# Performance work log

Measured on AMD Instinct MI355X. Metric: run time of the kernel, lower is better.

The kernel has to match this reference:

```python
import jax, jax.numpy as jnp
import numpy as np

CH = 512          # channels
HEADS = 8
HEAD_CH = 64
HIDDEN = HEADS * HEAD_CH  # 512
GROUPS = 32
EPS = 1e-5


def setup_inputs() -> dict:
    key = jax.random.key(0)
    ks = jax.random.split(key, 6)
    x = jax.random.normal(ks[0], (16, 32, 32, CH), dtype=jnp.float32)
    gn_scale = jnp.ones((CH,), dtype=jnp.float32)
    gn_offset = jnp.zeros((CH,), dtype=jnp.float32)
    w_qkv = jax.random.normal(ks[1], (CH, 3 * HIDDEN), dtype=jnp.float32) * 0.02
    # out_proj is zero-init in the original; use small random weights so the
    # residual branch is non-trivial for kernel correctness testing.
    w_out = jax.random.normal(ks[2], (HIDDEN, CH), dtype=jnp.float32) * 0.02
    b_out = jax.random.normal(ks[3], (CH,), dtype=jnp.float32) * 0.02
    return {"x": x, "gn_scale": gn_scale, "gn_offset": gn_offset,
            "w_qkv": w_qkv, "w_out": w_out, "b_out": b_out}


def group_norm(x, scale, offset):
    b, h, w, c = x.shape
    xg = x.reshape(b, h, w, GROUPS, c // GROUPS)
    mean = jnp.mean(xg, axis=(1, 2, 4), keepdims=True)
    var = jnp.var(xg, axis=(1, 2, 4), keepdims=True)
    xg = (xg - mean) * jax.lax.rsqrt(var + EPS)
    return xg.reshape(b, h, w, c) * scale + offset


def reference(x, gn_scale, gn_offset, w_qkv, w_out, b_out):
    b, h, w, c = x.shape
    n = h * w
    xn = jax.nn.silu(group_norm(x, gn_scale, gn_offset))
    qkv = jnp.einsum('bxyc,cd->bxyd', xn, w_qkv)  # [b,h,w,3*hidden]
    q, k, v = jnp.split(qkv, 3, axis=-1)
    # 'b x y (h c) -> b h c (x y)'
    def to_heads(a):
        a = a.reshape(b, n, HEADS, HEAD_CH)
        return jnp.transpose(a, (0, 2, 3, 1))  # b h d n
    q, k, v = to_heads(q), to_heads(k), to_heads(v)
    q = q * (HEAD_CH ** -0.5)
    sim = jnp.einsum('bhdi,bhdj->bhij', q, k)
    attn = jax.nn.softmax(sim, axis=-1)  # stable softmax (matches max-subtract)
    out = jnp.einsum('bhij,bhdj->bhid', attn, v)  # b h n d
    # 'b h (x y) d -> b x y (h d)'
    out = jnp.transpose(out, (0, 2, 1, 3)).reshape(b, h_ := h, w, HIDDEN) if False else \
          jnp.transpose(out, (0, 2, 1, 3)).reshape(b, h, w, HIDDEN)
    out = jnp.einsum('bxyd,dc->bxyc', out, w_out) + b_out
    return out + x
```

## Files before the change

### kernel.cpp

```cpp
#include <hip/hip_runtime.h>

#define BATCH 16
#define NPIX 1024
#define CH 512
#define HEADS 8
#define HD 64
#define GROUPS 32
#define CG 16
#define QKVW 1536

using bf16x8 = __attribute__((ext_vector_type(8))) short;
using f32x4  = __attribute__((ext_vector_type(4))) float;

__device__ inline unsigned short f2bf(float f) {
  unsigned int u = __builtin_bit_cast(unsigned int, f);
  u += 0x7fffu + ((u >> 16) & 1u);
  return (unsigned short)(u >> 16);
}

__device__ inline unsigned cvtpk(float lo, float hi) {
  unsigned r;
  asm("v_cvt_pk_bf16_f32 %0, %1, %2" : "=v"(r) : "v"(lo), "v"(hi));
  return r;
}

__device__ inline bf16x8 lds_frag(const unsigned short* S, int row, int slot) {
  return *(const bf16x8*)(S + row * 64 + (((slot ^ (row & 7)) << 3)));
}

__device__ inline void gload16(const unsigned short* g, unsigned short* l) {
  __builtin_amdgcn_global_load_lds(
      (const __attribute__((address_space(1))) unsigned int*)g,
      (__attribute__((address_space(3))) unsigned int*)l, 16, 0, 0);
}

__global__ __launch_bounds__(256) void wconv_kernel(
    const float* __restrict__ src, unsigned short* __restrict__ dst,
    const int K, const int N, const int q_cols) {
  __shared__ float tile[64][65];
  const int nb = N >> 6;
  const int k0 = (blockIdx.x / nb) << 6, n0 = (blockIdx.x % nb) << 6;
  const int t = threadIdx.x;
  const int row = t >> 2, c0 = (t & 3) << 4;
#pragma unroll
  for (int j = 0; j < 4; ++j) {
    const float4 v = *reinterpret_cast<const float4*>(
        src + (size_t)(k0 + row) * N + n0 + c0 + j * 4);
    tile[row][c0 + j * 4 + 0] = v.x;
    tile[row][c0 + j * 4 + 1] = v.y;
    tile[row][c0 + j * 4 + 2] = v.z;
    tile[row][c0 + j * 4 + 3] = v.w;
  }
  __syncthreads();
  const int n = t >> 2, kc = (t & 3) << 4;
  const float s = ((n0 + n) < q_cols) ? (0.125f * 1.44269504f) : 1.f;
#pragma unroll
  for (int j = 0; j < 4; ++j) {
    ushort4 o;
    o.x = f2bf(tile[kc + j * 4 + 0][n] * s);
    o.y = f2bf(tile[kc + j * 4 + 1][n] * s);
    o.z = f2bf(tile[kc + j * 4 + 2][n] * s);
    o.w = f2bf(tile[kc + j * 4 + 3][n] * s);
    *reinterpret_cast<ushort4*>(dst + (size_t)(n0 + n) * K + k0 + kc + j * 4) = o;
  }
}

__global__ __launch_bounds__(256) void gn_silu_kernel(
    const float* __restrict__ x, const float* __restrict__ sc,
    const float* __restrict__ of, unsigned short* __restrict__ y) {
  const int b = blockIdx.x >> 5, g = blockIdx.x & 31;
  const size_t base = (size_t)b * NPIX * CH + (size_t)g * CG;
  const int t = threadIdx.x;

  float4 vv[16];
  float sum = 0.f, ssq = 0.f;
#pragma unroll
  for (int it = 0; it < 16; ++it) {
    const int e4 = t + 256 * it;
    const int p = e4 >> 2, c = (e4 & 3) * 4;
    vv[it] = *reinterpret_cast<const float4*>(x + base + (size_t)p * CH + c);
    sum += vv[it].x + vv[it].y + vv[it].z + vv[it].w;
    ssq += vv[it].x * vv[it].x + vv[it].y * vv[it].y +
           vv[it].z * vv[it].z + vv[it].w * vv[it].w;
  }
#pragma unroll
  for (int m = 32; m > 0; m >>= 1) {
    sum += __shfl_down(sum, m);
    ssq += __shfl_down(ssq, m);
  }
  __shared__ float rs[4], rq[4], mv[2];
  const int lane = t & 63, wid = t >> 6;
  if (lane == 0) { rs[wid] = sum; rq[wid] = ssq; }
  __syncthreads();
  if (t == 0) {
    const float s = rs[0] + rs[1] + rs[2] + rs[3];
    const float q = rq[0] + rq[1] + rq[2] + rq[3];
    const float mean = s * (1.f / 16384.f);
    const float var = q * (1.f / 16384.f) - mean * mean;
    mv[0] = mean;
    mv[1] = rsqrtf(var + 1e-5f);
  }
  __syncthreads();
  const float mean = mv[0], rstd = mv[1];

#pragma unroll
  for (int it = 0; it < 16; ++it) {
    const int e4 = t + 256 * it;
    const int p = e4 >> 2, c = (e4 & 3) * 4;
    const float4 s4 = *reinterpret_cast<const float4*>(sc + g * CG + c);
    const float4 o4 = *reinterpret_cast<const float4*>(of + g * CG + c);
    float r[4];
    r[0] = (vv[it].x - mean) * rstd * s4.x + o4.x;
    r[1] = (vv[it].y - mean) * rstd * s4.y + o4.y;
    r[2] = (vv[it].z - mean) * rstd * s4.z + o4.z;
    r[3] = (vv[it].w - mean) * rstd * s4.w + o4.w;
    ushort4 o;
    o.x = f2bf(r[0] / (1.f + __expf(-r[0])));
    o.y = f2bf(r[1] / (1.f + __expf(-r[1])));
    o.z = f2bf(r[2] / (1.f + __expf(-r[2])));
    o.w = f2bf(r[3] / (1.f + __expf(-r[3])));
    *reinterpret_cast<ushort4*>(y + base + (size_t)p * CH + c) = o;
  }
}

template <bool EPI>
__global__ __launch_bounds__(256) void gemm_bf16_kernel(
    const unsigned short* __restrict__ A, const unsigned short* __restrict__ BT,
    void* __restrict__ Cv, const int M, const int N,
    const float* __restrict__ bias, const float* __restrict__ resid,
    unsigned short* __restrict__ vT) {
  __shared__ unsigned short lds[16384];
  unsigned short* As = lds;
  unsigned short* Bs = lds + 8192;
  const int Kd = 512;
  const int t = threadIdx.x;
  int bid = blockIdx.x;
  { const int q = gridDim.x >> 3; bid = (bid & 7) * q + (bid >> 3); }
  const int nb = N >> 7;
  const int m0 = (bid / nb) << 7, n0 = (bid % nb) << 7;
  const int wv = t >> 6, lane = t & 63;
  const int wr = (wv >> 1) << 6, wc = (wv & 1) << 6;
  const int l15 = lane & 15, l4 = lane >> 4;
  const bool vmode = !EPI && (n0 >= 1024);

  const int srow = t >> 3, sslot = t & 7;
  const int gslot = sslot ^ (srow & 7);
  const unsigned short* ag = A + (size_t)(m0 + srow) * Kd + gslot * 8;
  const unsigned short* bg = BT + (size_t)(n0 + srow) * Kd + gslot * 8;
  unsigned short* aw = As + wv * 512;
  unsigned short* bw = Bs + wv * 512;

  f32x4 acc[4][4];
#pragma unroll
  for (int i = 0; i < 4; ++i)
#pragma unroll
    for (int j = 0; j < 4; ++j) acc[i][j] = {0.f, 0.f, 0.f, 0.f};

#pragma unroll
  for (int s = 0; s < 8; ++s) {
    const int k0 = s * 64;
#pragma unroll
    for (int i = 0; i < 4; ++i) {
      gload16(ag + (size_t)(32 * i) * Kd + k0, aw + i * 2048);
      gload16(bg + (size_t)(32 * i) * Kd + k0, bw + i * 2048);
    }
    __syncthreads();
#pragma unroll
    for (int kk = 0; kk < 2; ++kk) {
      bf16x8 af[4], bfr[4];
#pragma unroll
      for (int i = 0; i < 4; ++i) {
        af[i] = lds_frag(As, wr + i * 16 + l15, kk * 4 + l4);
        bfr[i] = lds_frag(Bs, wc + i * 16 + l15, kk * 4 + l4);
      }
      if (vmode) {
#pragma unroll
        for (int ni = 0; ni < 4; ++ni)
#pragma unroll
          for (int mi = 0; mi < 4; ++mi)
            acc[ni][mi] = __builtin_amdgcn_mfma_f32_16x16x32_bf16(
                bfr[ni], af[mi], acc[ni][mi], 0, 0, 0);
      } else {
#pragma unroll
        for (int mi = 0; mi < 4; ++mi)
#pragma unroll
          for (int ni = 0; ni < 4; ++ni)
            acc[mi][ni] = __builtin_amdgcn_mfma_f32_16x16x32_bf16(
                af[mi], bfr[ni], acc[mi][ni], 0, 0, 0);
      }
    }
    __syncthreads();
  }

  if (EPI) {
#pragma unroll
    for (int mi = 0; mi < 4; ++mi)
#pragma unroll
      for (int ni = 0; ni < 4; ++ni) {
        const int col = n0 + wc + ni * 16 + l15;
#pragma unroll
        for (int r = 0; r < 4; ++r) {
          const int row = m0 + wr + mi * 16 + l4 * 4 + r;
          const size_t idx = (size_t)row * N + col;
          ((float*)Cv)[idx] = acc[mi][ni][r] + bias[col] + resid[idx];
        }
      }
  } else {
    unsigned short* Ct = lds;
#pragma unroll
    for (int ii = 0; ii < 4; ++ii)
#pragma unroll
      for (int jj = 0; jj < 4; ++jj) {
        const int rb = vmode ? (wc + ii * 16 + l4 * 4) : (wr + ii * 16 + l4 * 4);
        const int col = vmode ? (wr + jj * 16 + l15) : (wc + jj * 16 + l15);
#pragma unroll
        for (int r = 0; r < 4; ++r) {
          const int row = rb + r;
          Ct[row * 128 + ((((col >> 3) ^ (row & 15))) << 3) + (col & 7)] =
              f2bf(acc[ii][jj][r]);
        }
      }
    __syncthreads();
    const int erow = t >> 4;
    const int eslot = t & 15;
    if (!vmode) {
#pragma unroll
      for (int j = 0; j < 8; ++j) {
        const int row = erow + 16 * j;
        const uint4 v = *reinterpret_cast<const uint4*>(
            Ct + row * 128 + ((eslot ^ (row & 15)) << 3));
        *reinterpret_cast<uint4*>(
            (unsigned short*)Cv + (size_t)(m0 + row) * N + n0 + eslot * 8) = v;
      }
    } else {
      const int bb = m0 >> 10;
#pragma unroll
      for (int j = 0; j < 8; ++j) {
        const int row = erow + 16 * j;
        const uint4 v = *reinterpret_cast<const uint4*>(
            Ct + row * 128 + ((eslot ^ (row & 15)) << 3));
        *reinterpret_cast<uint4*>(
            vT + (((size_t)(bb * 512 + (n0 - 1024) + row)) << 10) +
            (m0 & 1023) + eslot * 8) = v;
      }
    }
  }
}

__global__ __launch_bounds__(256) void attn_mfma_kernel(
    const unsigned short* __restrict__ qkv, const unsigned short* __restrict__ vT,
    unsigned short* __restrict__ outb) {
  __shared__ unsigned short Ks[2][64 * 64];
  __shared__ unsigned short Vt[64 * 64];
  __shared__ unsigned short Ps[128 * 64];

  int bid = blockIdx.x;
  { const int q = gridDim.x >> 3; bid = (bid & 7) * q + (bid >> 3); }
  const int qt = bid & 7, h = (bid >> 3) & 7, b = bid >> 6;
  const int t = threadIdx.x, wv = t >> 6, lane = t & 63;
  const int l15 = lane & 15, l4 = lane >> 4;
  const int q0 = qt * 128;
  const size_t base = (size_t)b * NPIX * QKVW + h * HD;

  bf16x8 qf[2][2];
#pragma unroll
  for (int mi = 0; mi < 2; ++mi)
#pragma unroll
    for (int kk = 0; kk < 2; ++kk) {
      const int row = q0 + wv * 32 + mi * 16 + l15;
      qf[mi][kk] = *reinterpret_cast<const bf16x8*>(
          qkv + base + (size_t)row * QKVW + kk * 32 + l4 * 8);
    }

  f32x4 oaccT[4][2];
#pragma unroll
  for (int i = 0; i < 4; ++i)
#pragma unroll
    for (int j = 0; j < 2; ++j) oaccT[i][j] = {0.f, 0.f, 0.f, 0.f};
  float lrun[2] = {0.f, 0.f};

  const int srow = t >> 3, sslot = t & 7;
  const int gslot = sslot ^ (srow & 7);
  const unsigned short* kgp = qkv + base + 512 + (size_t)srow * QKVW + gslot * 8;
  const unsigned short* vgp =
      vT + (((size_t)(b * 512 + h * HD + srow)) << 10) + gslot * 8;
  unsigned short* kw[2] = {&Ks[0][0] + wv * 512, &Ks[1][0] + wv * 512};
  unsigned short* vw = &Vt[0] + wv * 512;

#pragma unroll
  for (int i = 0; i < 2; ++i) {
    gload16(kgp + (size_t)(32 * i) * QKVW, kw[0] + i * 2048);
    gload16(vgp + ((size_t)(32 * i) << 10), vw + i * 2048);
    gload16(kgp + (size_t)(64 + 32 * i) * QKVW, kw[1] + i * 2048);
  }
  __syncthreads();

  for (int kt = 0; kt < 16; ++kt) {
    const int cur = kt & 1;

    f32x4 sacc[4][2];
#pragma unroll
    for (int i = 0; i < 4; ++i)
#pragma unroll
      for (int j = 0; j < 2; ++j) sacc[i][j] = {0.f, 0.f, 0.f, 0.f};
    __builtin_amdgcn_s_setprio(1);
#pragma unroll
    for (int kk = 0; kk < 2; ++kk) {
      bf16x8 kf[4];
#pragma unroll
      for (int ni = 0; ni < 4; ++ni)
        kf[ni] = lds_frag(&Ks[cur][0], ni * 16 + l15, kk * 4 + l4);
#pragma unroll
      for (int ni = 0; ni < 4; ++ni)
#pragma unroll
        for (int mi = 0; mi < 2; ++mi)
          sacc[ni][mi] = __builtin_amdgcn_mfma_f32_16x16x32_bf16(
              kf[ni], qf[mi][kk], sacc[ni][mi], 0, 0, 0);
    }
    __builtin_amdgcn_s_setprio(0);

#pragma unroll
    for (int mi = 0; mi < 2; ++mi) {
      const int prow = wv * 32 + mi * 16 + l15;
      float rsum = 0.f;
#pragma unroll
      for (int ni = 0; ni < 4; ++ni) {
        float p[4];
#pragma unroll
        for (int r = 0; r < 4; ++r) {
          p[r] = exp2f(sacc[ni][mi][r]);
          rsum += p[r];
        }
        uint2 pw;
        pw.x = cvtpk(p[0], p[1]);
        pw.y = cvtpk(p[2], p[3]);
        const int slot = ni * 2 + (l4 >> 1);
        *reinterpret_cast<uint2*>(
            Ps + prow * 64 + ((slot ^ (prow & 7)) << 3) + ((l4 & 1) << 2)) = pw;
      }
      rsum += __shfl_xor(rsum, 16);
      rsum += __shfl_xor(rsum, 32);
      lrun[mi] += rsum;
    }

    __syncthreads();

    __builtin_amdgcn_s_setprio(1);
#pragma unroll
    for (int kk = 0; kk < 2; ++kk) {
      bf16x8 vf[4], pf[2];
#pragma unroll
      for (int dn = 0; dn < 4; ++dn)
        vf[dn] = lds_frag(&Vt[0], dn * 16 + l15, kk * 4 + l4);
#pragma unroll
      for (int mi = 0; mi < 2; ++mi)
        pf[mi] = lds_frag(Ps, wv * 32 + mi * 16 + l15, kk * 4 + l4);
#pragma unroll
      for (int dn = 0; dn < 4; ++dn)
#pragma unroll
        for (int mi = 0; mi < 2; ++mi)
          oaccT[dn][mi] = __builtin_amdgcn_mfma_f32_16x16x32_bf16(
              vf[dn], pf[mi], oaccT[dn][mi], 0, 0, 0);
    }
    __builtin_amdgcn_s_setprio(0);

    __syncthreads();

    if (kt < 15) {
      const int n0v = (kt + 1) * 64;
#pragma unroll
      for (int i = 0; i < 2; ++i)
        gload16(vgp + ((size_t)(32 * i) << 10) + n0v, vw + i * 2048);
      if (kt < 14) {
        const int n0k = (kt + 2) * 64;
#pragma unroll
        for (int i = 0; i < 2; ++i)
          gload16(kgp + (size_t)(n0k + 32 * i) * QKVW, kw[cur] + i * 2048);
      }
    }
  }

#pragma unroll
  for (int mi = 0; mi < 2; ++mi) {
    const float inv = 1.f / lrun[mi];
    const size_t n = (size_t)b * NPIX + q0 + wv * 32 + mi * 16 + l15;
#pragma unroll
    for (int dn = 0; dn < 4; ++dn) {
      uint2 o;
      o.x = cvtpk(oaccT[dn][mi][0] * inv, oaccT[dn][mi][1] * inv);
      o.y = cvtpk(oaccT[dn][mi][2] * inv, oaccT[dn][mi][3] * inv);
      *reinterpret_cast<uint2*>(outb + n * CH + h * HD + dn * 16 + l4 * 4) = o;
    }
  }
}

extern "C" void kernel_launch(void* const* d_in, const int* in_sizes, int n_in,
                              void* d_out, int out_size, void* d_ws, size_t ws_size,
                              hipStream_t stream) {
  const float* x = (const float*)d_in[0];
  const float* gsc = (const float*)d_in[1];
  const float* gof = (const float*)d_in[2];
  const float* wqkv = (const float*)d_in[3];
  const float* wout = (const float*)d_in[4];
  const float* bout = (const float*)d_in[5];
  float* out = (float*)d_out;

  unsigned short* qkvb = (unsigned short*)d_ws;
  unsigned short* xnb = qkvb + (size_t)16384 * 1536;
  unsigned short* wqT = xnb + (size_t)16384 * 512;
  unsigned short* woT = wqT + (size_t)1536 * 512;
  unsigned short* vTb = woT + (size_t)512 * 512;
  const size_t need = ((size_t)16384 * 1536 + (size_t)16384 * 512 +
                       (size_t)1536 * 512 + (size_t)512 * 512 +
                       (size_t)16 * 512 * 1024) * 2;
  if (ws_size < need) return;

  wconv_kernel<<<(512 / 64) * (1536 / 64), 256, 0, stream>>>(
      wqkv, wqT, 512, 1536, 512);
  wconv_kernel<<<(512 / 64) * (512 / 64), 256, 0, stream>>>(
      wout, woT, 512, 512, 0);
  gn_silu_kernel<<<BATCH * GROUPS, 256, 0, stream>>>(x, gsc, gof, xnb);
  gemm_bf16_kernel<false><<<(16384 / 128) * (1536 / 128), 256, 0, stream>>>(
      xnb, wqT, qkvb, 16384, 1536, nullptr, nullptr, vTb);
  attn_mfma_kernel<<<BATCH * HEADS * 8, 256, 0, stream>>>(qkvb, vTb, xnb);
  gemm_bf16_kernel<true><<<(16384 / 128) * (512 / 128), 256, 0, stream>>>(
      xnb, woT, out, 16384, 512, bout, x, nullptr);
}
```

Baseline: 154.8 us.

## Load K/V fragments directly from global memory, dropping LDS staging and block barriers

After: 207.2 us. 33.9% more time.

```diff
diff --git a/kernel.cpp b/kernel.cpp
--- a/kernel.cpp
+++ b/kernel.cpp
@@ -250,8 +250,6 @@
 __global__ __launch_bounds__(256) void attn_mfma_kernel(
     const unsigned short* __restrict__ qkv, const unsigned short* __restrict__ vT,
     unsigned short* __restrict__ outb) {
-  __shared__ unsigned short Ks[2][64 * 64];
-  __shared__ unsigned short Vt[64 * 64];
   __shared__ unsigned short Ps[128 * 64];
 
   int bid = blockIdx.x;
@@ -272,6 +270,10 @@
           qkv + base + (size_t)row * QKVW + kk * 32 + l4 * 8);
     }
 
+  const unsigned short* kfb = qkv + base + 512 + (size_t)l15 * QKVW + l4 * 8;
+  const unsigned short* vfb =
+      vT + (((size_t)(b * 512 + h * HD + l15)) << 10) + l4 * 8;
+
   f32x4 oaccT[4][2];
 #pragma unroll
   for (int i = 0; i < 4; ++i)
@@ -279,24 +281,16 @@
     for (int j = 0; j < 2; ++j) oaccT[i][j] = {0.f, 0.f, 0.f, 0.f};
   float lrun[2] = {0.f, 0.f};
 
-  const int srow = t >> 3, sslot = t & 7;
-  const int gslot = sslot ^ (srow & 7);
-  const unsigned short* kgp = qkv + base + 512 + (size_t)srow * QKVW + gslot * 8;
-  const unsigned short* vgp =
-      vT + (((size_t)(b * 512 + h * HD + srow)) << 10) + gslot * 8;
-  unsigned short* kw[2] = {&Ks[0][0] + wv * 512, &Ks[1][0] + wv * 512};
-  unsigned short* vw = &Vt[0] + wv * 512;
-
-#pragma unroll
-  for (int i = 0; i < 2; ++i) {
-    gload16(kgp + (size_t)(32 * i) * QKVW, kw[0] + i * 2048);
-    gload16(vgp + ((size_t)(32 * i) << 10), vw + i * 2048);
-    gload16(kgp + (size_t)(64 + 32 * i) * QKVW, kw[1] + i * 2048);
-  }
-  __syncthreads();
-
   for (int kt = 0; kt < 16; ++kt) {
-    const int cur = kt & 1;
+    const int n0k = kt * 64;
+
+    bf16x8 kf[2][4];
+#pragma unroll
+    for (int kk = 0; kk < 2; ++kk)
+#pragma unroll
+      for (int ni = 0; ni < 4; ++ni)
+        kf[kk][ni] = *reinterpret_cast<const bf16x8*>(
+            kfb + (size_t)(n0k + ni * 16) * QKVW + kk * 32);
 
     f32x4 sacc[4][2];
 #pragma unroll
@@ -305,19 +299,22 @@
       for (int j = 0; j < 2; ++j) sacc[i][j] = {0.f, 0.f, 0.f, 0.f};
     __builtin_amdgcn_s_setprio(1);
 #pragma unroll
-    for (int kk = 0; kk < 2; ++kk) {
-      bf16x8 kf[4];
-#pragma unroll
-      for (int ni = 0; ni < 4; ++ni)
-        kf[ni] = lds_frag(&Ks[cur][0], ni * 16 + l15, kk * 4 + l4);
+    for (int kk = 0; kk < 2; ++kk)
 #pragma unroll
       for (int ni = 0; ni < 4; ++ni)
 #pragma unroll
         for (int mi = 0; mi < 2; ++mi)
           sacc[ni][mi] = __builtin_amdgcn_mfma_f32_16x16x32_bf16(
-              kf[ni], qf[mi][kk], sacc[ni][mi], 0, 0, 0);
-    }
+              kf[kk][ni], qf[mi][kk], sacc[ni][mi], 0, 0, 0);
     __builtin_amdgcn_s_setprio(0);
+
+    bf16x8 vf[2][4];
+#pragma unroll
+    for (int kk = 0; kk < 2; ++kk)
+#pragma unroll
+      for (int dn = 0; dn < 4; ++dn)
+        vf[kk][dn] = *reinterpret_cast<const bf16x8*>(
+            vfb + (((size_t)(dn * 16)) << 10) + n0k + kk * 32);
 
 #pragma unroll
     for (int mi = 0; mi < 2; ++mi) {
@@ -343,15 +340,13 @@
       lrun[mi] += rsum;
     }
 
-    __syncthreads();
+    asm volatile("s_waitcnt lgkmcnt(0)" ::: "memory");
+    __builtin_amdgcn_sched_barrier(0);
 
     __builtin_amdgcn_s_setprio(1);
 #pragma unroll
     for (int kk = 0; kk < 2; ++kk) {
-      bf16x8 vf[4], pf[2];
-#pragma unroll
-      for (int dn = 0; dn < 4; ++dn)
-        vf[dn] = lds_frag(&Vt[0], dn * 16 + l15, kk * 4 + l4);
+      bf16x8 pf[2];
 #pragma unroll
       for (int mi = 0; mi < 2; ++mi)
         pf[mi] = lds_frag(Ps, wv * 32 + mi * 16 + l15, kk * 4 + l4);
@@ -360,24 +355,9 @@
 #pragma unroll
         for (int mi = 0; mi < 2; ++mi)
           oaccT[dn][mi] = __builtin_amdgcn_mfma_f32_16x16x32_bf16(
-              vf[dn], pf[mi], oaccT[dn][mi], 0, 0, 0);
+              vf[kk][dn], pf[mi], oaccT[dn][mi], 0, 0, 0);
     }
     __builtin_amdgcn_s_setprio(0);
-
-    __syncthreads();
-
-    if (kt < 15) {
-      const int n0v = (kt + 1) * 64;
-#pragma unroll
-      for (int i = 0; i < 2; ++i)
-        gload16(vgp + ((size_t)(32 * i) << 10) + n0v, vw + i * 2048);
-      if (kt < 14) {
-        const int n0k = (kt + 2) * 64;
-#pragma unroll
-        for (int i = 0; i < 2; ++i)
-          gload16(kgp + (size_t)(n0k + 32 * i) * QKVW, kw[cur] + i * 2048);
-      }
-    }
   }
 
 #pragma unroll
```

## Use 32x32 MFMA with register-resident P and double-buffered V in attention

Applied to the files above, without the earlier changes.

New measurement: 149.3 us. 1.04x faster.

```diff
diff --git a/kernel.cpp b/kernel.cpp
--- a/kernel.cpp
+++ b/kernel.cpp
@@ -11,6 +11,7 @@
 
 using bf16x8 = __attribute__((ext_vector_type(8))) short;
 using f32x4  = __attribute__((ext_vector_type(4))) float;
+using f32x16 = __attribute__((ext_vector_type(16))) float;
 
 __device__ inline unsigned short f2bf(float f) {
   unsigned int u = __builtin_bit_cast(unsigned int, f);
@@ -251,33 +252,28 @@
     const unsigned short* __restrict__ qkv, const unsigned short* __restrict__ vT,
     unsigned short* __restrict__ outb) {
   __shared__ unsigned short Ks[2][64 * 64];
-  __shared__ unsigned short Vt[64 * 64];
-  __shared__ unsigned short Ps[128 * 64];
+  __shared__ unsigned short Vt[2][64 * 64];
 
   int bid = blockIdx.x;
   { const int q = gridDim.x >> 3; bid = (bid & 7) * q + (bid >> 3); }
   const int qt = bid & 7, h = (bid >> 3) & 7, b = bid >> 6;
   const int t = threadIdx.x, wv = t >> 6, lane = t & 63;
-  const int l15 = lane & 15, l4 = lane >> 4;
-  const int q0 = qt * 128;
+  const int l31 = lane & 31, hi = lane >> 5;
+  const int q0 = qt * 128 + wv * 32;
   const size_t base = (size_t)b * NPIX * QKVW + h * HD;
 
-  bf16x8 qf[2][2];
-#pragma unroll
-  for (int mi = 0; mi < 2; ++mi)
-#pragma unroll
-    for (int kk = 0; kk < 2; ++kk) {
-      const int row = q0 + wv * 32 + mi * 16 + l15;
-      qf[mi][kk] = *reinterpret_cast<const bf16x8*>(
-          qkv + base + (size_t)row * QKVW + kk * 32 + l4 * 8);
-    }
-
-  f32x4 oaccT[4][2];
-#pragma unroll
-  for (int i = 0; i < 4; ++i)
-#pragma unroll
-    for (int j = 0; j < 2; ++j) oaccT[i][j] = {0.f, 0.f, 0.f, 0.f};
-  float lrun[2] = {0.f, 0.f};
+  bf16x8 qf[4];
+#pragma unroll
+  for (int dk = 0; dk < 4; ++dk)
+    qf[dk] = *reinterpret_cast<const bf16x8*>(
+        qkv + base + (size_t)(q0 + l31) * QKVW + dk * 16 + hi * 8);
+
+  f32x16 oacc[2];
+#pragma unroll
+  for (int i = 0; i < 2; ++i)
+#pragma unroll
+    for (int r = 0; r < 16; ++r) oacc[i][r] = 0.f;
+  float lrun = 0.f;
 
   const int srow = t >> 3, sslot = t & 7;
   const int gslot = sslot ^ (srow & 7);
@@ -285,113 +281,96 @@
   const unsigned short* vgp =
       vT + (((size_t)(b * 512 + h * HD + srow)) << 10) + gslot * 8;
   unsigned short* kw[2] = {&Ks[0][0] + wv * 512, &Ks[1][0] + wv * 512};
-  unsigned short* vw = &Vt[0] + wv * 512;
+  unsigned short* vw[2] = {&Vt[0][0] + wv * 512, &Vt[1][0] + wv * 512};
 
 #pragma unroll
   for (int i = 0; i < 2; ++i) {
     gload16(kgp + (size_t)(32 * i) * QKVW, kw[0] + i * 2048);
-    gload16(vgp + ((size_t)(32 * i) << 10), vw + i * 2048);
+    gload16(vgp + ((size_t)(32 * i) << 10), vw[0] + i * 2048);
     gload16(kgp + (size_t)(64 + 32 * i) * QKVW, kw[1] + i * 2048);
+    gload16(vgp + ((size_t)(32 * i) << 10) + 64, vw[1] + i * 2048);
   }
   __syncthreads();
 
   for (int kt = 0; kt < 16; ++kt) {
     const int cur = kt & 1;
 
-    f32x4 sacc[4][2];
-#pragma unroll
-    for (int i = 0; i < 4; ++i)
-#pragma unroll
-      for (int j = 0; j < 2; ++j) sacc[i][j] = {0.f, 0.f, 0.f, 0.f};
+    f32x16 sacc[2];
+#pragma unroll
+    for (int i = 0; i < 2; ++i)
+#pragma unroll
+      for (int r = 0; r < 16; ++r) sacc[i][r] = 0.f;
     __builtin_amdgcn_s_setprio(1);
 #pragma unroll
-    for (int kk = 0; kk < 2; ++kk) {
-      bf16x8 kf[4];
-#pragma unroll
-      for (int ni = 0; ni < 4; ++ni)
-        kf[ni] = lds_frag(&Ks[cur][0], ni * 16 + l15, kk * 4 + l4);
-#pragma unroll
-      for (int ni = 0; ni < 4; ++ni)
-#pragma unroll
-        for (int mi = 0; mi < 2; ++mi)
-          sacc[ni][mi] = __builtin_amdgcn_mfma_f32_16x16x32_bf16(
-              kf[ni], qf[mi][kk], sacc[ni][mi], 0, 0, 0);
-    }
+    for (int kb = 0; kb < 2; ++kb)
+#pragma unroll
+      for (int dk = 0; dk < 4; ++dk) {
+        const bf16x8 kf = lds_frag(&Ks[cur][0], kb * 32 + l31, dk * 2 + hi);
+        sacc[kb] = __builtin_amdgcn_mfma_f32_32x32x16_bf16(
+            kf, qf[dk], sacc[kb], 0, 0, 0);
+      }
     __builtin_amdgcn_s_setprio(0);
 
-#pragma unroll
-    for (int mi = 0; mi < 2; ++mi) {
-      const int prow = wv * 32 + mi * 16 + l15;
-      float rsum = 0.f;
-#pragma unroll
-      for (int ni = 0; ni < 4; ++ni) {
-        float p[4];
-#pragma unroll
-        for (int r = 0; r < 4; ++r) {
-          p[r] = exp2f(sacc[ni][mi][r]);
-          rsum += p[r];
-        }
-        uint2 pw;
-        pw.x = cvtpk(p[0], p[1]);
-        pw.y = cvtpk(p[2], p[3]);
-        const int slot = ni * 2 + (l4 >> 1);
-        *reinterpret_cast<uint2*>(
-            Ps + prow * 64 + ((slot ^ (prow & 7)) << 3) + ((l4 & 1) << 2)) = pw;
-      }
-      rsum += __shfl_xor(rsum, 16);
-      rsum += __shfl_xor(rsum, 32);
-      lrun[mi] += rsum;
-    }
+    float rsum = 0.f;
+#pragma unroll
+    for (int kb = 0; kb < 2; ++kb)
+#pragma unroll
+      for (int r = 0; r < 16; ++r) {
+        sacc[kb][r] = exp2f(sacc[kb][r]);
+        rsum += sacc[kb][r];
+      }
+    rsum += __shfl_xor(rsum, 32);
+    lrun += rsum;
+
+    bf16x8 pf[4];
+#pragma unroll
+    for (int kk = 0; kk < 4; ++kk) {
+      const int kb = kk >> 1, ra = (kk & 1) << 3;
+      unsigned u = cvtpk(sacc[kb][ra + 0], sacc[kb][ra + 1]);
+      unsigned w = cvtpk(sacc[kb][ra + 4], sacc[kb][ra + 5]);
+      unsigned v = cvtpk(sacc[kb][ra + 2], sacc[kb][ra + 3]);
+      unsigned x = cvtpk(sacc[kb][ra + 6], sacc[kb][ra + 7]);
+      asm("v_permlane32_swap_b32 %0, %1" : "+v"(u), "+v"(w));
+      asm("v_permlane32_swap_b32 %0, %1" : "+v"(v), "+v"(x));
+      uint4 pw = {u, v, w, x};
+      pf[kk] = __builtin_bit_cast(bf16x8, pw);
+    }
+
+    __builtin_amdgcn_s_setprio(1);
+#pragma unroll
+    for (int db = 0; db < 2; ++db)
+#pragma unroll
+      for (int kk = 0; kk < 4; ++kk) {
+        const bf16x8 vf = lds_frag(&Vt[cur][0], db * 32 + l31, kk * 2 + hi);
+        oacc[db] = __builtin_amdgcn_mfma_f32_32x32x16_bf16(
+            vf, pf[kk], oacc[db], 0, 0, 0);
+      }
+    __builtin_amdgcn_s_setprio(0);
 
     __syncthreads();
 
-    __builtin_amdgcn_s_setprio(1);
-#pragma unroll
-    for (int kk = 0; kk < 2; ++kk) {
-      bf16x8 vf[4], pf[2];
-#pragma unroll
-      for (int dn = 0; dn < 4; ++dn)
-        vf[dn] = lds_frag(&Vt[0], dn * 16 + l15, kk * 4 + l4);
-#pragma unroll
-      for (int mi = 0; mi < 2; ++mi)
-        pf[mi] = lds_frag(Ps, wv * 32 + mi * 16 + l15, kk * 4 + l4);
-#pragma unroll
-      for (int dn = 0; dn < 4; ++dn)
-#pragma unroll
-        for (int mi = 0; mi < 2; ++mi)
-          oaccT[dn][mi] = __builtin_amdgcn_mfma_f32_16x16x32_bf16(
-              vf[dn], pf[mi], oaccT[dn][mi], 0, 0, 0);
-    }
-    __builtin_amdgcn_s_setprio(0);
-
-    __syncthreads();
-
-    if (kt < 15) {
-      const int n0v = (kt + 1) * 64;
-#pragma unroll
-      for (int i = 0; i < 2; ++i)
-        gload16(vgp + ((size_t)(32 * i) << 10) + n0v, vw + i * 2048);
-      if (kt < 14) {
-        const int n0k = (kt + 2) * 64;
-#pragma unroll
-        for (int i = 0; i < 2; ++i)
-          gload16(kgp + (size_t)(n0k + 32 * i) * QKVW, kw[cur] + i * 2048);
-      }
-    }
-  }
-
-#pragma unroll
-  for (int mi = 0; mi < 2; ++mi) {
-    const float inv = 1.f / lrun[mi];
-    const size_t n = (size_t)b * NPIX + q0 + wv * 32 + mi * 16 + l15;
-#pragma unroll
-    for (int dn = 0; dn < 4; ++dn) {
+    if (kt < 14) {
+      const int n0n = (kt + 2) * 64;
+#pragma unroll
+      for (int i = 0; i < 2; ++i) {
+        gload16(kgp + (size_t)(n0n + 32 * i) * QKVW, kw[cur] + i * 2048);
+        gload16(vgp + ((size_t)(32 * i) << 10) + n0n, vw[cur] + i * 2048);
+      }
+    }
+  }
+
+  const float inv = 1.f / lrun;
+  const size_t n = (size_t)b * NPIX + q0 + l31;
+#pragma unroll
+  for (int db = 0; db < 2; ++db)
+#pragma unroll
+    for (int rq = 0; rq < 4; ++rq) {
       uint2 o;
-      o.x = cvtpk(oaccT[dn][mi][0] * inv, oaccT[dn][mi][1] * inv);
-      o.y = cvtpk(oaccT[dn][mi][2] * inv, oaccT[dn][mi][3] * inv);
-      *reinterpret_cast<uint2*>(outb + n * CH + h * HD + dn * 16 + l4 * 4) = o;
-    }
-  }
+      o.x = cvtpk(oacc[db][rq * 4 + 0] * inv, oacc[db][rq * 4 + 1] * inv);
+      o.y = cvtpk(oacc[db][rq * 4 + 2] * inv, oacc[db][rq * 4 + 3] * inv);
+      *reinterpret_cast<uint2*>(
+          outb + n * CH + h * HD + db * 32 + rq * 8 + hi * 4) = o;
+    }
 }
 
 extern "C" void kernel_launch(void* const* d_in, const int* in_sizes, int n_in,
```
